# Kernel optimization log

Measured on AMD Instinct MI355X. Metric: run time of the kernel, lower is better.

Reference implementation:

```python
import jax, jax.numpy as jnp
import numpy as np

N_BLOCKS = 16
N_HEADS = 2
HEAD_DIM = 32
SCALE = HEAD_DIM ** (-0.5)


def setup_inputs() -> dict:
    key = jax.random.key(0)
    ks = jax.random.split(key, 5)
    b, s, d = 16, 4096, 1024
    nb, bd = N_BLOCKS, 1024 // N_BLOCKS  # block_dim = 64; emb per-block dim = 64
    w_std = 1.0 / np.sqrt(bd)
    inp = {
        'x': jax.random.normal(ks[0], (b, s, d), dtype=jnp.float32),
        'wq': jax.random.normal(ks[1], (nb, bd, bd), dtype=jnp.float32) * w_std,
        'bq': jnp.zeros((nb, bd), dtype=jnp.float32),
        'wk': jax.random.normal(ks[2], (nb, bd, bd), dtype=jnp.float32) * w_std,
        'bk': jnp.zeros((nb, bd), dtype=jnp.float32),
        'wv': jax.random.normal(ks[3], (nb, bd, bd), dtype=jnp.float32) * w_std,
        'bv': jnp.zeros((nb, bd), dtype=jnp.float32),
        'wf': jax.random.normal(ks[4], (nb, bd, bd), dtype=jnp.float32) * w_std,
        'bf': jnp.zeros((nb, bd), dtype=jnp.float32),
    }
    return inp


def _group_linear(x, w, b):
    # x: [B, S, G*I] -> per-block linear -> [B, S, G*O]
    B, S, _ = x.shape
    G, I, O = w.shape
    xg = x.reshape(B, S, G, I)
    y = jnp.einsum('bsgi,gio->bsgo', xg, w) + b
    return y.reshape(B, S, G * O)


def reference(x, wq, bq, wk, bk, wv, bv, wf, bf):
    B, S, D = x.shape
    nb, nh, hd = N_BLOCKS, N_HEADS, HEAD_DIM
    # grouped QKV projections -> [B, S, nb, nh, hd] -> heads before blocks
    q = _group_linear(x, wq, bq).reshape(B, S, nb, nh, hd).transpose(0, 1, 3, 2, 4) * SCALE
    k = _group_linear(x, wk, bk).reshape(B, S, nb, nh, hd).transpose(0, 1, 3, 2, 4)
    v = _group_linear(x, wv, bv).reshape(B, S, nb, nh, hd).transpose(0, 1, 3, 2, 4)
    # attention across blocks: score [B, S, nh, nb, nb]
    score = jnp.einsum('bshgd,bshfd->bshgf', q, k)
    score = jax.nn.softmax(score, axis=-1)
    out = jnp.einsum('bshgf,bshfd->bshgd', score, v)
    # back to [B, S, nb, nh, hd] then flatten
    out = out.transpose(0, 1, 3, 2, 4).reshape(B, S, nb * nh * hd)
    out = _group_linear(out, wf, bf)
    return out.reshape(B, S, D)
```

## Files before the change

### kernel.cpp

```cpp
#include <hip/hip_runtime.h>
#include <hip/hip_bf16.h>
#include <stdint.h>


typedef __attribute__((ext_vector_type(8))) short bf16x8;
typedef __attribute__((ext_vector_type(4))) float f32x4;

#define NTOK   65536
#define DM     1024
#define TT     16
#define QSCALE 0.17677669529663687f
#define LOG2E  1.4426950408889634f

static __device__ __forceinline__ unsigned short f2bf(float f) {
  union { __hip_bfloat16 h; unsigned short s; } cv;
  cv.h = __float2bfloat16(f);
  return cv.s;
}

static __device__ __forceinline__ unsigned int pk2(float a, float b) {
  return (unsigned int)f2bf(a) | ((unsigned int)f2bf(b) << 16);
}

static __device__ __forceinline__ bf16x8 pack8(float4 a, float4 b) {
  bf16x8 r;
  r[0] = (short)f2bf(a.x); r[1] = (short)f2bf(a.y);
  r[2] = (short)f2bf(a.z); r[3] = (short)f2bf(a.w);
  r[4] = (short)f2bf(b.x); r[5] = (short)f2bf(b.y);
  r[6] = (short)f2bf(b.z); r[7] = (short)f2bf(b.w);
  return r;
}

union FragCast { uint4 u4; bf16x8 v; uint2 u2[2]; unsigned int u[4]; };

__global__ void build_wfrag(const float* __restrict__ wq, const float* __restrict__ wk,
                            const float* __restrict__ wv, const float* __restrict__ wf,
                            uint4* __restrict__ wfrag) {
  int tid = blockIdx.x * 256 + threadIdx.x;
  if (tid >= 4 * 16 * 2 * 4 * 64) return;
  int lane =  tid        & 63;
  int nf   = (tid >> 6)  & 3;
  int kk   = (tid >> 8)  & 1;
  int g    = (tid >> 9)  & 15;
  int mat  =  tid >> 13;
  const float* w = (mat == 0) ? wq : (mat == 1) ? wk : (mat == 2) ? wv : wf;
  float sc = (mat == 0) ? QSCALE : 1.0f;
  int o  = nf * 16 + (lane & 15);
  int kb = kk * 32 + 8 * (lane >> 4);
  unsigned int packed[4];
#pragma unroll
  for (int jj = 0; jj < 4; ++jj) {
    unsigned short lo = f2bf(w[(g * 64 + kb + 2 * jj    ) * 64 + o] * sc);
    unsigned short hi = f2bf(w[(g * 64 + kb + 2 * jj + 1) * 64 + o] * sc);
    packed[jj] = (unsigned int)lo | ((unsigned int)hi << 16);
  }
  uint4 u; u.x = packed[0]; u.y = packed[1]; u.z = packed[2]; u.w = packed[3];
  wfrag[tid] = u;
}


#define QK_ONE(fA_, fB_, nf2_, h_, bp_, bsc_, dst_) do {                      \
  const int nf = 2 * (h_) + (nf2_);                                           \
  float4 b4 = *(const float4*)&(bp_)[g * 64 + nf * 16 + 4 * lq];              \
  f32x4 a1 = {b4.x * (bsc_), b4.y * (bsc_), b4.z * (bsc_), b4.w * (bsc_)};    \
  a1 = __builtin_amdgcn_mfma_f32_16x16x32_bf16((fA_).v, afr0, a1, 0, 0, 0);   \
  a1 = __builtin_amdgcn_mfma_f32_16x16x32_bf16((fB_).v, afr1, a1, 0, 0, 0);   \
  uint2 w2; w2.x = pk2(a1[0], a1[1]); w2.y = pk2(a1[2], a1[3]);               \
  const int blk = (16 * (2 * (nf2_) + (lq >> 1)) + g) ^ (lr & 7);             \
  *(uint2*)&(dst_)[lr * 512 + blk * 8 + 4 * (lq & 1)] = w2;                   \
} while (0)

#define V_ONE(fA_, fB_, nf2_, h_) do {                                        \
  const int nf = 2 * (h_) + (nf2_);                                           \
  const float bias = bv[g * 64 + nf * 16 + lr];                               \
  f32x4 a1 = {bias, bias, bias, bias};                                        \
  a1 = __builtin_amdgcn_mfma_f32_16x16x32_bf16(afr0, (fA_).v, a1, 0, 0, 0);   \
  a1 = __builtin_amdgcn_mfma_f32_16x16x32_bf16(afr1, (fB_).v, a1, 0, 0, 0);   \
  const int L = 16 * (g >> 2) + lr;                                           \
  const int jj = g & 3;                                                       \
  _Pragma("unroll")                                                           \
  for (int r = 0; r < 4; ++r)                                                 \
    s_v[((4 * lq + r) * 2 + (nf2_)) * 256 + L * 4 + jj] = f2bf(a1[r]);        \
} while (0)

#define PH1(h_) do {                                                          \
  {                                                                           \
    FragCast qa0, qb0, qa1, qb1;                            \
    qa0.u4 = wfrag[(((0 * 16 + g) * 2 + 0) * 4 + 2 * (h_)    ) * 64 + lane];  \
    qb0.u4 = wfrag[(((0 * 16 + g) * 2 + 0) * 4 + 2 * (h_) + 1) * 64 + lane];  \
    qa1.u4 = wfrag[(((0 * 16 + g) * 2 + 1) * 4 + 2 * (h_)    ) * 64 + lane];  \
    qb1.u4 = wfrag[(((0 * 16 + g) * 2 + 1) * 4 + 2 * (h_) + 1) * 64 + lane];  \
    QK_ONE(qa0, qa1, 0, h_, bq, QSCALE, s_q);                                 \
    QK_ONE(qb0, qb1, 1, h_, bq, QSCALE, s_q);                                 \
  }                                                                           \
  {                                                                           \
    FragCast ka0, kb0, ka1, kb1;                                              \
    ka0.u4 = wfrag[(((1 * 16 + g) * 2 + 0) * 4 + 2 * (h_)    ) * 64 + lane];  \
    kb0.u4 = wfrag[(((1 * 16 + g) * 2 + 0) * 4 + 2 * (h_) + 1) * 64 + lane];  \
    ka1.u4 = wfrag[(((1 * 16 + g) * 2 + 1) * 4 + 2 * (h_)    ) * 64 + lane];  \
    kb1.u4 = wfrag[(((1 * 16 + g) * 2 + 1) * 4 + 2 * (h_) + 1) * 64 + lane];  \
    QK_ONE(ka0, ka1, 0, h_, bk, 1.0f, s_k);                                   \
    QK_ONE(kb0, kb1, 1, h_, bk, 1.0f, s_k);                                   \
  }                                                                           \
  {                                                                           \
    FragCast va0, vb0, va1, vb1;                                              \
    va0.u4 = wfrag[(((2 * 16 + g) * 2 + 0) * 4 + 2 * (h_)    ) * 64 + lane];  \
    vb0.u4 = wfrag[(((2 * 16 + g) * 2 + 0) * 4 + 2 * (h_) + 1) * 64 + lane];  \
    va1.u4 = wfrag[(((2 * 16 + g) * 2 + 1) * 4 + 2 * (h_)    ) * 64 + lane];  \
    vb1.u4 = wfrag[(((2 * 16 + g) * 2 + 1) * 4 + 2 * (h_) + 1) * 64 + lane];  \
    V_ONE(va0, va1, 0, h_);                                                   \
    V_ONE(vb0, vb1, 1, h_);                                                   \
  }                                                                           \
} while (0)

#define PH2() do {                                                            \
  const int t = g;                                                            \
  f32x4 zero = {0.f, 0.f, 0.f, 0.f};                                          \
  FragCast qa, ka;                                                            \
  const int blk = lane ^ (t & 7);                                             \
  qa.u4 = *(const uint4*)&s_q[t * 512 + blk * 8];                             \
  ka.u4 = *(const uint4*)&s_k[t * 512 + blk * 8];                             \
                  \
  f32x4 sc4 = __builtin_amdgcn_mfma_f32_16x16x32_bf16(ka.v, qa.v, zero, 0, 0, 0); \
  float m = fmaxf(fmaxf(sc4[0], sc4[1]), fmaxf(sc4[2], sc4[3]));              \
  m = fmaxf(m, __shfl_xor(m, 16));                                            \
  m = fmaxf(m, __shfl_xor(m, 32));                                            \
  float p0 = exp2f((sc4[0] - m) * LOG2E);                                     \
  float p1 = exp2f((sc4[1] - m) * LOG2E);                                     \
  float p2 = exp2f((sc4[2] - m) * LOG2E);                                     \
  float p3 = exp2f((sc4[3] - m) * LOG2E);                                     \
  float s = p0 + p1 + p2 + p3;                                                \
  s += __shfl_xor(s, 16);                                                     \
  s += __shfl_xor(s, 32);                                                     \
  const float inv = __fdividef(1.0f, s);                                      \
  FragCast pa;                        \
  pa.u[0] = pk2(p0 * inv, p1 * inv);                                          \
  pa.u[1] = pk2(p2 * inv, p3 * inv);                                          \
  pa.u[2] = 0; pa.u[3] = 0;                                                   \
  FragCast va0, va1;            \
  va0.u2[0] = *(const uint2*)&s_v[(t * 2 + 0) * 256 + lane * 4];              \
  va0.u[2] = 0; va0.u[3] = 0;                                                 \
  va1.u2[0] = *(const uint2*)&s_v[(t * 2 + 1) * 256 + lane * 4];              \
  va1.u[2] = 0; va1.u[3] = 0;                                                 \
                                   \
  f32x4 oo0 = __builtin_amdgcn_mfma_f32_16x16x32_bf16(va0.v, pa.v, zero, 0, 0, 0); \
  f32x4 oo1 = __builtin_amdgcn_mfma_f32_16x16x32_bf16(va1.v, pa.v, zero, 0, 0, 0); \
  uint2 w20; w20.x = pk2(oo0[0], oo0[1]); w20.y = pk2(oo0[2], oo0[3]);        \
  const int ab0 = (16 * (0 + (lq >> 1)) + lr) ^ (t & 7);                      \
  *(uint2*)&s_att[t * 512 + ab0 * 8 + 4 * (lq & 1)] = w20;                    \
  uint2 w21; w21.x = pk2(oo1[0], oo1[1]); w21.y = pk2(oo1[2], oo1[3]);        \
  const int ab1 = (16 * (2 + (lq >> 1)) + lr) ^ (t & 7);                      \
  *(uint2*)&s_att[t * 512 + ab1 * 8 + 4 * (lq & 1)] = w21;                    \
} while (0)

#define PH3(h_) do {                                                          \
  FragCast f0, f1, f2, f3;                                                    \
  f0.u4 = wfrag[(((3 * 16 + g) * 2 + (h_)) * 4 + 0) * 64 + lane];             \
  f1.u4 = wfrag[(((3 * 16 + g) * 2 + (h_)) * 4 + 1) * 64 + lane];             \
  f2.u4 = wfrag[(((3 * 16 + g) * 2 + (h_)) * 4 + 2) * 64 + lane];             \
  f3.u4 = wfrag[(((3 * 16 + g) * 2 + (h_)) * 4 + 3) * 64 + lane];             \
  const int blk3 = (16 * lq + g) ^ (lr & 7);                                  \
  FragCast aa;                        \
  aa.u4 = *(const uint4*)&s_att[lr * 512 + blk3 * 8];                         \
  acc0 = __builtin_amdgcn_mfma_f32_16x16x32_bf16(f0.v, aa.v, acc0, 0, 0, 0);  \
  acc1 = __builtin_amdgcn_mfma_f32_16x16x32_bf16(f1.v, aa.v, acc1, 0, 0, 0);  \
  acc2 = __builtin_amdgcn_mfma_f32_16x16x32_bf16(f2.v, aa.v, acc2, 0, 0, 0);  \
  acc3 = __builtin_amdgcn_mfma_f32_16x16x32_bf16(f3.v, aa.v, acc3, 0, 0, 0);  \
} while (0)

__global__ __launch_bounds__(1024, 8)
void fused_gc16(const float* __restrict__ x,
                const float* __restrict__ bq, const float* __restrict__ bk,
                const float* __restrict__ bv, const float* __restrict__ bfb,
                const uint4* __restrict__ wfrag,
                float* __restrict__ out) {
  __shared__ __align__(16) unsigned short s_q  [16 * 512];
  __shared__ __align__(16) unsigned short s_k  [16 * 512];
  __shared__ __align__(16) unsigned short s_v  [16 * 2 * 256];
  __shared__ __align__(16) unsigned short s_att[16 * 512];

  const int tid  = threadIdx.x;
  const int g    = tid >> 6;
  const int lane = tid & 63;
  const int lr   = lane & 15;
  const int lq   = lane >> 4;
  const long tok0 = (long)blockIdx.x * TT;

  bf16x8 afr0, afr1;
  {
    const float* xr = x + (tok0 + lr) * DM + g * 64;
    afr0 = pack8(*(const float4*)(xr + 8 * lq), *(const float4*)(xr + 8 * lq + 4));
    afr1 = pack8(*(const float4*)(xr + 32 + 8 * lq), *(const float4*)(xr + 32 + 8 * lq + 4));
  }

  f32x4 acc0, acc1, acc2, acc3;

  PH1(0);
  __syncthreads();
  PH2();
  __syncthreads();
  {
    float4 b0 = *(const float4*)&bfb[g * 64 +  0 + 4 * lq];
    float4 b1 = *(const float4*)&bfb[g * 64 + 16 + 4 * lq];
    float4 b2 = *(const float4*)&bfb[g * 64 + 32 + 4 * lq];
    float4 b3 = *(const float4*)&bfb[g * 64 + 48 + 4 * lq];
    acc0[0] = b0.x; acc0[1] = b0.y; acc0[2] = b0.z; acc0[3] = b0.w;
    acc1[0] = b1.x; acc1[1] = b1.y; acc1[2] = b1.z; acc1[3] = b1.w;
    acc2[0] = b2.x; acc2[1] = b2.y; acc2[2] = b2.z; acc2[3] = b2.w;
    acc3[0] = b3.x; acc3[1] = b3.y; acc3[2] = b3.z; acc3[3] = b3.w;
  }
  PH3(0);
  PH1(1);
  __syncthreads();
  PH2();
  __syncthreads();
  PH3(1);

  {
    float* orow = out + (tok0 + lr) * DM + g * 64 + 4 * lq;
    float4 o4;
    o4.x = acc0[0]; o4.y = acc0[1]; o4.z = acc0[2]; o4.w = acc0[3];
    *(float4*)(orow +  0) = o4;
    o4.x = acc1[0]; o4.y = acc1[1]; o4.z = acc1[2]; o4.w = acc1[3];
    *(float4*)(orow + 16) = o4;
    o4.x = acc2[0]; o4.y = acc2[1]; o4.z = acc2[2]; o4.w = acc2[3];
    *(float4*)(orow + 32) = o4;
    o4.x = acc3[0]; o4.y = acc3[1]; o4.z = acc3[2]; o4.w = acc3[3];
    *(float4*)(orow + 48) = o4;
  }
}

extern "C" void kernel_launch(void* const* d_in, const int* in_sizes, int n_in,
                              void* d_out, int out_size, void* d_ws, size_t ws_size,
                              hipStream_t stream) {
  const float* x   = (const float*)d_in[0];
  const float* wq  = (const float*)d_in[1];
  const float* bq_ = (const float*)d_in[2];
  const float* wk  = (const float*)d_in[3];
  const float* bk_ = (const float*)d_in[4];
  const float* wv  = (const float*)d_in[5];
  const float* bv_ = (const float*)d_in[6];
  const float* wf  = (const float*)d_in[7];
  const float* bf_ = (const float*)d_in[8];
  (void)in_sizes; (void)n_in; (void)out_size; (void)ws_size;

  uint4* wfrag = (uint4*)d_ws;

  build_wfrag<<<128, 256, 0, stream>>>(wq, wk, wv, wf, wfrag);
  fused_gc16<<<NTOK / TT, 1024, 0, stream>>>(x, bq_, bk_, bv_, bf_, wfrag,
                                             (float*)d_out);
}
```

Baseline: 238.8 us.

## Double-buffer attention output and defer final projection to a single pass

Measured after the change: 259.7 us. 1.09x slower.

```diff
diff --git a/kernel.cpp b/kernel.cpp
--- a/kernel.cpp
+++ b/kernel.cpp
@@ -59,7 +59,7 @@
 }
 
 
-#define QK_ONE(fA_, fB_, nf2_, h_, bp_, bsc_, dst_) do {                      \
+#define QK_STORE(fA_, fB_, nf2_, h_, bp_, bsc_, dst_) do {                    \
   const int nf = 2 * (h_) + (nf2_);                                           \
   float4 b4 = *(const float4*)&(bp_)[g * 64 + nf * 16 + 4 * lq];              \
   f32x4 a1 = {b4.x * (bsc_), b4.y * (bsc_), b4.z * (bsc_), b4.w * (bsc_)};    \
@@ -70,50 +70,42 @@
   *(uint2*)&(dst_)[lr * 512 + blk * 8 + 4 * (lq & 1)] = w2;                   \
 } while (0)
 
-#define V_ONE(fA_, fB_, nf2_, h_) do {                                        \
+#define V_STORE(fA_, fB_, nf2_, h_) do {                                      \
   const int nf = 2 * (h_) + (nf2_);                                           \
   const float bias = bv[g * 64 + nf * 16 + lr];                               \
+  const int L = 16 * (g >> 2) + lr;                                           \
+  const int jj = g & 3;                                                       \
   f32x4 a1 = {bias, bias, bias, bias};                                        \
   a1 = __builtin_amdgcn_mfma_f32_16x16x32_bf16(afr0, (fA_).v, a1, 0, 0, 0);   \
   a1 = __builtin_amdgcn_mfma_f32_16x16x32_bf16(afr1, (fB_).v, a1, 0, 0, 0);   \
-  const int L = 16 * (g >> 2) + lr;                                           \
-  const int jj = g & 3;                                                       \
   _Pragma("unroll")                                                           \
   for (int r = 0; r < 4; ++r)                                                 \
     s_v[((4 * lq + r) * 2 + (nf2_)) * 256 + L * 4 + jj] = f2bf(a1[r]);        \
 } while (0)
 
 #define PH1(h_) do {                                                          \
-  {                                                                           \
-    FragCast qa0, qb0, qa1, qb1;                            \
-    qa0.u4 = wfrag[(((0 * 16 + g) * 2 + 0) * 4 + 2 * (h_)    ) * 64 + lane];  \
-    qb0.u4 = wfrag[(((0 * 16 + g) * 2 + 0) * 4 + 2 * (h_) + 1) * 64 + lane];  \
-    qa1.u4 = wfrag[(((0 * 16 + g) * 2 + 1) * 4 + 2 * (h_)    ) * 64 + lane];  \
-    qb1.u4 = wfrag[(((0 * 16 + g) * 2 + 1) * 4 + 2 * (h_) + 1) * 64 + lane];  \
-    QK_ONE(qa0, qa1, 0, h_, bq, QSCALE, s_q);                                 \
-    QK_ONE(qb0, qb1, 1, h_, bq, QSCALE, s_q);                                 \
-  }                                                                           \
-  {                                                                           \
-    FragCast ka0, kb0, ka1, kb1;                                              \
-    ka0.u4 = wfrag[(((1 * 16 + g) * 2 + 0) * 4 + 2 * (h_)    ) * 64 + lane];  \
-    kb0.u4 = wfrag[(((1 * 16 + g) * 2 + 0) * 4 + 2 * (h_) + 1) * 64 + lane];  \
-    ka1.u4 = wfrag[(((1 * 16 + g) * 2 + 1) * 4 + 2 * (h_)    ) * 64 + lane];  \
-    kb1.u4 = wfrag[(((1 * 16 + g) * 2 + 1) * 4 + 2 * (h_) + 1) * 64 + lane];  \
-    QK_ONE(ka0, ka1, 0, h_, bk, 1.0f, s_k);                                   \
-    QK_ONE(kb0, kb1, 1, h_, bk, 1.0f, s_k);                                   \
-  }                                                                           \
-  {                                                                           \
-    FragCast va0, vb0, va1, vb1;                                              \
-    va0.u4 = wfrag[(((2 * 16 + g) * 2 + 0) * 4 + 2 * (h_)    ) * 64 + lane];  \
-    vb0.u4 = wfrag[(((2 * 16 + g) * 2 + 0) * 4 + 2 * (h_) + 1) * 64 + lane];  \
-    va1.u4 = wfrag[(((2 * 16 + g) * 2 + 1) * 4 + 2 * (h_)    ) * 64 + lane];  \
-    vb1.u4 = wfrag[(((2 * 16 + g) * 2 + 1) * 4 + 2 * (h_) + 1) * 64 + lane];  \
-    V_ONE(va0, va1, 0, h_);                                                   \
-    V_ONE(vb0, vb1, 1, h_);                                                   \
-  }                                                                           \
-} while (0)
-
-#define PH2() do {                                                            \
+  FragCast q0a, q0b, q1a, q1b, k0a, k0b, k1a, k1b, v0a, v0b, v1a, v1b;        \
+  q0a.u4 = wfrag[(((0 * 16 + g) * 2 + 0) * 4 + 2 * (h_)    ) * 64 + lane];    \
+  q0b.u4 = wfrag[(((0 * 16 + g) * 2 + 1) * 4 + 2 * (h_)    ) * 64 + lane];    \
+  q1a.u4 = wfrag[(((0 * 16 + g) * 2 + 0) * 4 + 2 * (h_) + 1) * 64 + lane];    \
+  q1b.u4 = wfrag[(((0 * 16 + g) * 2 + 1) * 4 + 2 * (h_) + 1) * 64 + lane];    \
+  k0a.u4 = wfrag[(((1 * 16 + g) * 2 + 0) * 4 + 2 * (h_)    ) * 64 + lane];    \
+  k0b.u4 = wfrag[(((1 * 16 + g) * 2 + 1) * 4 + 2 * (h_)    ) * 64 + lane];    \
+  k1a.u4 = wfrag[(((1 * 16 + g) * 2 + 0) * 4 + 2 * (h_) + 1) * 64 + lane];    \
+  k1b.u4 = wfrag[(((1 * 16 + g) * 2 + 1) * 4 + 2 * (h_) + 1) * 64 + lane];    \
+  v0a.u4 = wfrag[(((2 * 16 + g) * 2 + 0) * 4 + 2 * (h_)    ) * 64 + lane];    \
+  v0b.u4 = wfrag[(((2 * 16 + g) * 2 + 1) * 4 + 2 * (h_)    ) * 64 + lane];    \
+  v1a.u4 = wfrag[(((2 * 16 + g) * 2 + 0) * 4 + 2 * (h_) + 1) * 64 + lane];    \
+  v1b.u4 = wfrag[(((2 * 16 + g) * 2 + 1) * 4 + 2 * (h_) + 1) * 64 + lane];    \
+  QK_STORE(q0a, q0b, 0, h_, bq, QSCALE, s_q);                                 \
+  QK_STORE(q1a, q1b, 1, h_, bq, QSCALE, s_q);                                 \
+  QK_STORE(k0a, k0b, 0, h_, bk, 1.0f,   s_k);                                 \
+  QK_STORE(k1a, k1b, 1, h_, bk, 1.0f,   s_k);                                 \
+  V_STORE(v0a, v0b, 0, h_);                                                   \
+  V_STORE(v1a, v1b, 1, h_);                                                   \
+} while (0)
+
+#define PH2(ATT_) do {                                                        \
   const int t = g;                                                            \
   f32x4 zero = {0.f, 0.f, 0.f, 0.f};                                          \
   FragCast qa, ka;                                                            \
@@ -147,37 +139,54 @@
   f32x4 oo1 = __builtin_amdgcn_mfma_f32_16x16x32_bf16(va1.v, pa.v, zero, 0, 0, 0); \
   uint2 w20; w20.x = pk2(oo0[0], oo0[1]); w20.y = pk2(oo0[2], oo0[3]);        \
   const int ab0 = (16 * (0 + (lq >> 1)) + lr) ^ (t & 7);                      \
-  *(uint2*)&s_att[t * 512 + ab0 * 8 + 4 * (lq & 1)] = w20;                    \
+  *(uint2*)&(ATT_)[t * 512 + ab0 * 8 + 4 * (lq & 1)] = w20;                   \
   uint2 w21; w21.x = pk2(oo1[0], oo1[1]); w21.y = pk2(oo1[2], oo1[3]);        \
   const int ab1 = (16 * (2 + (lq >> 1)) + lr) ^ (t & 7);                      \
-  *(uint2*)&s_att[t * 512 + ab1 * 8 + 4 * (lq & 1)] = w21;                    \
-} while (0)
-
-#define PH3(h_) do {                                                          \
-  FragCast f0, f1, f2, f3;                                                    \
-  f0.u4 = wfrag[(((3 * 16 + g) * 2 + (h_)) * 4 + 0) * 64 + lane];             \
-  f1.u4 = wfrag[(((3 * 16 + g) * 2 + (h_)) * 4 + 1) * 64 + lane];             \
-  f2.u4 = wfrag[(((3 * 16 + g) * 2 + (h_)) * 4 + 2) * 64 + lane];             \
-  f3.u4 = wfrag[(((3 * 16 + g) * 2 + (h_)) * 4 + 3) * 64 + lane];             \
+  *(uint2*)&(ATT_)[t * 512 + ab1 * 8 + 4 * (lq & 1)] = w21;                   \
+} while (0)
+
+#define LOADF() do {                                                          \
+  f0n0.u4 = wfrag[(((3 * 16 + g) * 2 + 0) * 4 + 0) * 64 + lane];              \
+  f0n1.u4 = wfrag[(((3 * 16 + g) * 2 + 0) * 4 + 1) * 64 + lane];              \
+  f0n2.u4 = wfrag[(((3 * 16 + g) * 2 + 0) * 4 + 2) * 64 + lane];              \
+  f0n3.u4 = wfrag[(((3 * 16 + g) * 2 + 0) * 4 + 3) * 64 + lane];              \
+  f1n0.u4 = wfrag[(((3 * 16 + g) * 2 + 1) * 4 + 0) * 64 + lane];              \
+  f1n1.u4 = wfrag[(((3 * 16 + g) * 2 + 1) * 4 + 1) * 64 + lane];              \
+  f1n2.u4 = wfrag[(((3 * 16 + g) * 2 + 1) * 4 + 2) * 64 + lane];              \
+  f1n3.u4 = wfrag[(((3 * 16 + g) * 2 + 1) * 4 + 3) * 64 + lane];              \
+} while (0)
+
+#define PH3_NF(f0_, f1_, nf_, aa0_, aa1_) do {                                \
+  float4 b4 = *(const float4*)&bfb[g * 64 + (nf_) * 16 + 4 * lq];             \
+  f32x4 a1 = {b4.x, b4.y, b4.z, b4.w};                                        \
+  a1 = __builtin_amdgcn_mfma_f32_16x16x32_bf16((f0_).v, (aa0_).v, a1, 0, 0, 0); \
+  a1 = __builtin_amdgcn_mfma_f32_16x16x32_bf16((f1_).v, (aa1_).v, a1, 0, 0, 0); \
+  float4 o4; o4.x = a1[0]; o4.y = a1[1]; o4.z = a1[2]; o4.w = a1[3];          \
+  *(float4*)&out[(tok0 + lr) * DM + g * 64 + (nf_) * 16 + 4 * lq] = o4;       \
+} while (0)
+
+#define PH3() do {                                                            \
   const int blk3 = (16 * lq + g) ^ (lr & 7);                                  \
-  FragCast aa;                        \
-  aa.u4 = *(const uint4*)&s_att[lr * 512 + blk3 * 8];                         \
-  acc0 = __builtin_amdgcn_mfma_f32_16x16x32_bf16(f0.v, aa.v, acc0, 0, 0, 0);  \
-  acc1 = __builtin_amdgcn_mfma_f32_16x16x32_bf16(f1.v, aa.v, acc1, 0, 0, 0);  \
-  acc2 = __builtin_amdgcn_mfma_f32_16x16x32_bf16(f2.v, aa.v, acc2, 0, 0, 0);  \
-  acc3 = __builtin_amdgcn_mfma_f32_16x16x32_bf16(f3.v, aa.v, acc3, 0, 0, 0);  \
-} while (0)
-
-__global__ __launch_bounds__(1024, 8)
-void fused_gc16(const float* __restrict__ x,
-                const float* __restrict__ bq, const float* __restrict__ bk,
-                const float* __restrict__ bv, const float* __restrict__ bfb,
-                const uint4* __restrict__ wfrag,
-                float* __restrict__ out) {
-  __shared__ __align__(16) unsigned short s_q  [16 * 512];
-  __shared__ __align__(16) unsigned short s_k  [16 * 512];
-  __shared__ __align__(16) unsigned short s_v  [16 * 2 * 256];
-  __shared__ __align__(16) unsigned short s_att[16 * 512];
+  FragCast aa0, aa1;                   \
+  aa0.u4 = *(const uint4*)&s_a0[lr * 512 + blk3 * 8];                         \
+  aa1.u4 = *(const uint4*)&s_a1[lr * 512 + blk3 * 8];                         \
+  PH3_NF(f0n0, f1n0, 0, aa0, aa1);                                            \
+  PH3_NF(f0n1, f1n1, 1, aa0, aa1);                                            \
+  PH3_NF(f0n2, f1n2, 2, aa0, aa1);                                            \
+  PH3_NF(f0n3, f1n3, 3, aa0, aa1);                                            \
+} while (0)
+
+__global__ __launch_bounds__(1024)
+void fused_gc16b(const float* __restrict__ x,
+                 const float* __restrict__ bq, const float* __restrict__ bk,
+                 const float* __restrict__ bv, const float* __restrict__ bfb,
+                 const uint4* __restrict__ wfrag,
+                 float* __restrict__ out) {
+  __shared__ __align__(16) unsigned short s_q [16 * 512];
+  __shared__ __align__(16) unsigned short s_k [16 * 512];
+  __shared__ __align__(16) unsigned short s_v [16 * 512];
+  __shared__ __align__(16) unsigned short s_a0[16 * 512];
+  __shared__ __align__(16) unsigned short s_a1[16 * 512];
 
   const int tid  = threadIdx.x;
   const int g    = tid >> 6;
@@ -193,41 +202,18 @@
     afr1 = pack8(*(const float4*)(xr + 32 + 8 * lq), *(const float4*)(xr + 32 + 8 * lq + 4));
   }
 
-  f32x4 acc0, acc1, acc2, acc3;
+  FragCast f0n0, f0n1, f0n2, f0n3, f1n0, f1n1, f1n2, f1n3;
 
   PH1(0);
   __syncthreads();
-  PH2();
-  __syncthreads();
-  {
-    float4 b0 = *(const float4*)&bfb[g * 64 +  0 + 4 * lq];
-    float4 b1 = *(const float4*)&bfb[g * 64 + 16 + 4 * lq];
-    float4 b2 = *(const float4*)&bfb[g * 64 + 32 + 4 * lq];
-    float4 b3 = *(const float4*)&bfb[g * 64 + 48 + 4 * lq];
-    acc0[0] = b0.x; acc0[1] = b0.y; acc0[2] = b0.z; acc0[3] = b0.w;
-    acc1[0] = b1.x; acc1[1] = b1.y; acc1[2] = b1.z; acc1[3] = b1.w;
-    acc2[0] = b2.x; acc2[1] = b2.y; acc2[2] = b2.z; acc2[3] = b2.w;
-    acc3[0] = b3.x; acc3[1] = b3.y; acc3[2] = b3.z; acc3[3] = b3.w;
-  }
-  PH3(0);
+  PH2(s_a0);
+  __syncthreads();
   PH1(1);
   __syncthreads();
-  PH2();
-  __syncthreads();
-  PH3(1);
-
-  {
-    float* orow = out + (tok0 + lr) * DM + g * 64 + 4 * lq;
-    float4 o4;
-    o4.x = acc0[0]; o4.y = acc0[1]; o4.z = acc0[2]; o4.w = acc0[3];
-    *(float4*)(orow +  0) = o4;
-    o4.x = acc1[0]; o4.y = acc1[1]; o4.z = acc1[2]; o4.w = acc1[3];
-    *(float4*)(orow + 16) = o4;
-    o4.x = acc2[0]; o4.y = acc2[1]; o4.z = acc2[2]; o4.w = acc2[3];
-    *(float4*)(orow + 32) = o4;
-    o4.x = acc3[0]; o4.y = acc3[1]; o4.z = acc3[2]; o4.w = acc3[3];
-    *(float4*)(orow + 48) = o4;
-  }
+  LOADF();
+  PH2(s_a1);
+  __syncthreads();
+  PH3();
 }
 
 extern "C" void kernel_launch(void* const* d_in, const int* in_sizes, int n_in,
@@ -247,6 +233,6 @@
   uint4* wfrag = (uint4*)d_ws;
 
   build_wfrag<<<128, 256, 0, stream>>>(wq, wk, wv, wf, wfrag);
-  fused_gc16<<<NTOK / TT, 1024, 0, stream>>>(x, bq_, bk_, bv_, bf_, wfrag,
-                                             (float*)d_out);
-}
+  fused_gc16b<<<NTOK / TT, 1024, 0, stream>>>(x, bq_, bk_, bv_, bf_, wfrag,
+                                              (float*)d_out);
+}
```
